# Kernel optimization log

Measured on AMD Instinct MI355X. Metric: run time of the kernel, lower is better.

## Reference

```python
import jax, jax.numpy as jnp
import numpy as np

B, S, V, D, H, L = 4, 1024, 32000, 256, 8, 4
DH = D // H  # per-head dim (D_H == F_H since F=D)
EPS = 1e-5


def _layernorm(x, g, b):
    m = jnp.mean(x, axis=-1, keepdims=True)
    v = jnp.mean((x - m) ** 2, axis=-1, keepdims=True)
    return (x - m) * jax.lax.rsqrt(v + EPS) * g + b


def _forward(X, emb, WQ, WK, WV, O, ln_g, ln_b, w1, b1, w2, b2, w3, b3, logitW):
    x = emb[X]  # [B,S,D]
    scale = 1.0 / np.sqrt(DH).astype(np.float32)
    nlayers = WQ.shape[0]
    for i in range(nlayers):
        xn = _layernorm(x, ln_g[i], ln_b[i])
        xh = xn.reshape(B, S, H, DH)  # [B,S,H,DH]
        # repeated 'dd'/'ff' indices extract the DIAGONAL of the per-head weights
        scores = jnp.einsum('bqhd,hdd,bkhd,hdd->bhqk', xh, WQ[i], xh, WK[i]) * scale
        attn = jax.nn.softmax(scores, axis=-1)  # [B,H,S,S]
        y = jnp.einsum('bhqk,bkhf,hff->bqhf', attn, xh, WV[i]).reshape(B, S, D)
        y = jnp.einsum('bqf,ff->bqf', y, O[i])  # diagonal output scaling
        y = jax.nn.gelu(y @ w1[i] + b1[i], approximate=False)
        y = jax.nn.gelu(y @ w2[i] + b2[i], approximate=False)
        y = y @ w3[i] + b3[i]
        x = x + y
    return jnp.einsum('bqd,dt->bqt', x, logitW)  # [B,S,V]


def setup_inputs() -> dict:
    key = jax.random.key(0)
    ks = jax.random.split(key, 16)

    def xavier(k, shape, fan_in, fan_out):
        std = np.sqrt(2.0 / (fan_in + fan_out)).astype(np.float32)
        return jax.random.normal(k, shape, jnp.float32) * std

    inp = {
        'X': jax.random.randint(ks[0], (B, S), 0, V, dtype=jnp.int64),
        'emb': jax.random.normal(ks[1], (V, D), jnp.float32),
        'WQ': xavier(ks[2], (L, H, DH, DH), DH, DH),
        'WK': xavier(ks[3], (L, H, DH, DH), DH, DH),
        'WV': xavier(ks[4], (L, H, DH, DH), DH, DH),
        'O': xavier(ks[5], (L, D, D), D, D),
        'ln_g': jnp.ones((L, D), jnp.float32),
        'ln_b': jnp.zeros((L, D), jnp.float32),
        'w1': xavier(ks[6], (L, D, D), D, D),
        'b1': jnp.zeros((L, D), jnp.float32),
        'w2': xavier(ks[7], (L, D, D), D, D),
        'b2': jnp.zeros((L, D), jnp.float32),
        'w3': xavier(ks[8], (L, D, D), D, D),
        'b3': jnp.zeros((L, D), jnp.float32),
        'logitW': xavier(ks[9], (D, V), D, V),
    }
    return inp


def reference(X, emb, WQ, WK, WV, O, ln_g, ln_b, w1, b1, w2, b2, w3, b3, logitW):
    return _forward(X, emb, WQ, WK, WV, O, ln_g, ln_b, w1, b1, w2, b2, w3, b3, logitW)
```

## Files before the change

### kernel.cpp

```cpp
#include <hip/hip_runtime.h>
#include <hip/hip_bf16.h>
#include <cstdint>
#include <cstddef>

#define B_ 4
#define S_ 1024
#define V_ 32000
#define D_ 256
#define H_ 8
#define DH_ 32
#define L_ 4
#define MROWS (B_*S_)

typedef __attribute__((ext_vector_type(8))) short bf16x8;
typedef __attribute__((ext_vector_type(4))) float f32x4;

__device__ __forceinline__ unsigned short f2bf(float f) {
  union { float f; unsigned u; } c; c.f = f;
  unsigned u = c.u;
  u += 0x7fff + ((u >> 16) & 1);
  return (unsigned short)(u >> 16);
}
__device__ __forceinline__ float bf2f(unsigned short u) {
  union { unsigned u; float f; } c; c.u = ((unsigned)u) << 16; return c.f;
}

__device__ __forceinline__ void gload16(const unsigned short* g, unsigned short* l) {
  __builtin_amdgcn_global_load_lds(
      (const __attribute__((address_space(1))) void*)g,
      (__attribute__((address_space(3))) void*)l, 16, 0, 0);
}

template<int BM, int BK, int NW>
__device__ __forceinline__ void stage_tile_swz(const unsigned short* __restrict__ g, int ldg,
                                               unsigned short* lds, int wave, int lane) {
  constexpr int CH  = BM * BK * 2 / 1024;
  constexpr int BKB = BK * 2;
#pragma unroll
  for (int t = 0; t < CH / NW; ++t) {
    int c = wave + t * NW;
    int byte  = c * 1024 + lane * 16;
    int row   = byte / BKB;
    int inner = (byte % BKB) ^ ((row & 7) << 4);
    gload16(g + (size_t)row * ldg + (inner >> 1), lds + c * 512);
  }
}

template<int BKB>
__device__ __forceinline__ bf16x8 lds_frag(const unsigned short* base, int row, int kbytes) {
  int b = (row * BKB + kbytes) ^ ((row & 7) << 4);
  return *(const bf16x8*)((const char*)base + b);
}

__global__ __launch_bounds__(512) void k_prep(
    const int* __restrict__ X, const float* __restrict__ emb,
    const float* __restrict__ lng, const float* __restrict__ lnb,
    float* __restrict__ x, unsigned short* __restrict__ xbf,
    unsigned short* __restrict__ xnT,
    const float* __restrict__ w1, const float* __restrict__ w2,
    const float* __restrict__ w3, unsigned short* __restrict__ mlpW) {
  int tid = threadIdx.x;
  if (blockIdx.x < 256) {
    __shared__ __align__(16) float xf[16][264];
    __shared__ float mrow[16], rrow[16];
    int r0 = blockIdx.x * 16;
    int w = tid >> 6, lane = tid & 63;
#pragma unroll
    for (int rr = 0; rr < 2; rr++) {
      int row = w * 2 + rr; int grow = r0 + row;
      int tok = X[grow];
      f32x4 v = *(const f32x4*)(emb + (size_t)tok * D_ + lane * 4);
      *(f32x4*)(x + (size_t)grow * D_ + lane * 4) = v;
      *(f32x4*)&xf[row][lane * 4] = v;
      float s = v[0] + v[1] + v[2] + v[3];
      float ss = v[0]*v[0] + v[1]*v[1] + v[2]*v[2] + v[3]*v[3];
#pragma unroll
      for (int off = 1; off < 64; off <<= 1) {
        s  += __shfl_xor(s, off, 64);
        ss += __shfl_xor(ss, off, 64);
      }
      float mean = s * (1.f / D_);
      float var = ss * (1.f / D_) - mean * mean;
      float rinv = rsqrtf(var + 1e-5f);
      float4 g4 = *(const float4*)(lng + lane * 4);
      float4 b4 = *(const float4*)(lnb + lane * 4);
      ushort4 o;
      o.x = f2bf((v[0] - mean) * rinv * g4.x + b4.x);
      o.y = f2bf((v[1] - mean) * rinv * g4.y + b4.y);
      o.z = f2bf((v[2] - mean) * rinv * g4.z + b4.z);
      o.w = f2bf((v[3] - mean) * rinv * g4.w + b4.w);
      *(ushort4*)(xbf + (size_t)grow * D_ + lane * 4) = o;
      if (lane == 0) { mrow[row] = mean; rrow[row] = rinv; }
    }
    __syncthreads();
    int d = tid & 255, half = tid >> 8;
    float gd = lng[d], bd = lnb[d];
    int bb = r0 >> 10, s0 = r0 & 1023;
    bf16x8 o8;
#pragma unroll
    for (int k = 0; k < 8; k++) {
      int srow = half * 8 + k;
      o8[k] = (short)f2bf((xf[srow][d] - mrow[srow]) * rrow[srow] * gd + bd);
    }
    *(bf16x8*)(xnT + ((size_t)(bb * 256 + d)) * S_ + s0 + half * 8) = o8;
  } else {
    __shared__ float tile[64][65];
    int idx = blockIdx.x - 256;
    int z = idx >> 4;
    int rem = idx & 15;
    int r0 = (rem >> 2) * 64, c0 = (rem & 3) * 64;
    int l = z / 3, mm = z % 3;
    const float* in = (mm == 0 ? w1 : mm == 1 ? w2 : w3) + (size_t)l * 65536;
    unsigned short* out = mlpW + (size_t)z * 65536;
    int t = tid & 255;
    bool act = tid < 256;
    if (act) {
#pragma unroll
      for (int i = 0; i < 16; i++) {
        int id2 = i * 256 + t;
        int lr = id2 >> 6, lc = id2 & 63;
        tile[lr][lc] = in[(size_t)(r0 + lr) * 256 + c0 + lc];
      }
    }
    __syncthreads();
    if (act) {
#pragma unroll
      for (int i = 0; i < 16; i++) {
        int id2 = i * 256 + t;
        int lr = id2 >> 6, lc = id2 & 63;
        out[(size_t)(c0 + lr) * 256 + r0 + lc] = f2bf(tile[lc][lr]);
      }
    }
  }
}

template<int LAST>
__global__ __launch_bounds__(512) void k_layer(
    const unsigned short* __restrict__ xbf,
    const unsigned short* __restrict__ xnT,
    const float* __restrict__ WQ, const float* __restrict__ WK,
    const float* __restrict__ WV, const float* __restrict__ Om,
    const unsigned short* __restrict__ Wl,
    const float* __restrict__ b1, const float* __restrict__ b2, const float* __restrict__ b3,
    float* __restrict__ x,
    const float* __restrict__ lngN, const float* __restrict__ lnbN,
    unsigned short* __restrict__ xbfN, unsigned short* __restrict__ xnTN,
    unsigned short* __restrict__ actB,
    int layer) {
  __shared__ __align__(16) unsigned short P_lds[8][16][72];
  __shared__ __align__(16) unsigned short Aa[16 * 256];
  __shared__ __align__(16) unsigned short Ab[16 * 256];
  __shared__ __align__(16) unsigned short Ab2[16 * 256];
  __shared__ __align__(16) unsigned short Bp[3][256 * 64];
  __shared__ __align__(16) float xf[16][264];
  __shared__ float mrow[16], rrow[16];

  int b = blockIdx.x >> 6;
  int q0 = (blockIdx.x & 63) << 4;
  int r0 = blockIdx.x * 16;
  int tid = threadIdx.x;
  int w = tid >> 6, lane = tid & 63;
  int lr = lane & 15, lg = lane >> 4;
  int h = w;

  stage_tile_swz<256, 64, 8>(Wl, 256, Bp[0], w, lane);

  const float scale = 0.17677669529663687f;
  bf16x8 aq;
  {
    bf16x8 xq = *(const bf16x8*)(xbf + ((size_t)(b * S_ + q0 + lr)) * D_ + h * DH_ + lg * 8);
#pragma unroll
    for (int j = 0; j < 8; j++) {
      int dj = lg * 8 + j;
      float wq = WQ[((size_t)(layer * H_ + h)) * 1024 + dj * 33];
      float wk = WK[((size_t)(layer * H_ + h)) * 1024 + dj * 33];
      aq[j] = (short)f2bf(bf2f((unsigned short)xq[j]) * wq * wk * scale);
    }
  }
  float dvo[2];
#pragma unroll
  for (int fs = 0; fs < 2; fs++) {
    int fh = fs * 16 + lr;
    int fc = h * DH_ + fh;
    dvo[fs] = WV[((size_t)(layer * H_ + h)) * 1024 + fh * 33] *
              Om[(size_t)layer * 65536 + (size_t)fc * 257];
  }

  f32x4 accPV[2];
  accPV[0] = (f32x4){0.f, 0.f, 0.f, 0.f};
  accPV[1] = (f32x4){0.f, 0.f, 0.f, 0.f};
  float rsum[4] = {0.f, 0.f, 0.f, 0.f};

  const unsigned short* xk_base = xbf + ((size_t)b * S_) * D_ + h * DH_ + lg * 8;
  const unsigned short* vT_base = xnT + ((size_t)(b * D_ + h * DH_)) * S_;

  bf16x8 qkb[4];
#pragma unroll
  for (int c = 0; c < 4; c++)
    qkb[c] = *(const bf16x8*)(xk_base + (size_t)(c * 16 + lr) * D_);

  for (int kt = 0; kt < 16; kt++) {
    int k0 = kt * 64;
    bf16x8 pvb[2][2];
#pragma unroll
    for (int fs = 0; fs < 2; fs++)
#pragma unroll
      for (int kc = 0; kc < 2; kc++)
        pvb[fs][kc] = *(const bf16x8*)(vT_base + (size_t)(fs * 16 + lr) * S_ +
                                       k0 + kc * 32 + lg * 8);
    f32x4 s[4];
#pragma unroll
    for (int c = 0; c < 4; c++)
      s[c] = __builtin_amdgcn_mfma_f32_16x16x32_bf16(aq, qkb[c],
                (f32x4){0.f, 0.f, 0.f, 0.f}, 0, 0, 0);
    int ktn = kt < 15 ? kt + 1 : 15;
#pragma unroll
    for (int c = 0; c < 4; c++)
      qkb[c] = *(const bf16x8*)(xk_base + (size_t)(ktn * 64 + c * 16 + lr) * D_);
#pragma unroll
    for (int c = 0; c < 4; c++)
#pragma unroll
      for (int r = 0; r < 4; r++) {
        float p = __expf(s[c][r]);
        rsum[r] += p;
        P_lds[w][lg * 4 + r][c * 16 + lr] = f2bf(p);
      }
#pragma unroll
    for (int kc = 0; kc < 2; kc++) {
      bf16x8 pa = *(const bf16x8*)(&P_lds[w][lr][kc * 32 + lg * 8]);
#pragma unroll
      for (int fs = 0; fs < 2; fs++)
        accPV[fs] = __builtin_amdgcn_mfma_f32_16x16x32_bf16(pa, pvb[fs][kc],
                       accPV[fs], 0, 0, 0);
    }
  }

  float inv[4];
#pragma unroll
  for (int r = 0; r < 4; r++) {
    float v = rsum[r];
    v += __shfl_xor(v, 1, 64);
    v += __shfl_xor(v, 2, 64);
    v += __shfl_xor(v, 4, 64);
    v += __shfl_xor(v, 8, 64);
    inv[r] = 1.f / v;
  }
#pragma unroll
  for (int fs = 0; fs < 2; fs++)
#pragma unroll
    for (int r = 0; r < 4; r++) {
      float val = accPV[fs][r] * inv[r] * dvo[fs];
      int row = lg * 4 + r, col = h * DH_ + fs * 16 + lr;
      int byte = (row * 512 + col * 2) ^ ((row & 7) << 4);
      *(unsigned short*)((char*)Aa + byte) = f2bf(val);
    }
  __syncthreads();

  int lr16 = lr;
  f32x4 acc[2];
  acc[0] = (f32x4){0.f, 0.f, 0.f, 0.f};
  acc[1] = (f32x4){0.f, 0.f, 0.f, 0.f};
  const unsigned short* Asrc = Aa;

  stage_tile_swz<256, 64, 8>(Wl + 64, 256, Bp[1], w, lane);

  for (int p = 0; p < 12; ++p) {
    if (p < 10) {
      int pn = p + 2;
      stage_tile_swz<256, 64, 8>(Wl + (size_t)(pn >> 2) * 65536 + (pn & 3) * 64,
                                 256, Bp[pn % 3], w, lane);
    }
    int kk0 = (p & 3) * 64;
#pragma unroll
    for (int kk = 0; kk < 64; kk += 32) {
      bf16x8 a = lds_frag<512>(Asrc, lr16, (kk0 + kk) * 2 + lg * 16);
#pragma unroll
      for (int j = 0; j < 2; j++) {
        bf16x8 bfg = lds_frag<128>(Bp[p % 3], w * 32 + j * 16 + lr16, kk * 2 + lg * 16);
        acc[j] = __builtin_amdgcn_mfma_f32_16x16x32_bf16(a, bfg, acc[j], 0, 0, 0);
      }
    }
    if (p == 3 || p == 7) {
      const float* bias = (p == 3) ? b1 : b2;
      unsigned short* dst = (p == 3) ? Ab : Ab2;
#pragma unroll
      for (int j = 0; j < 2; j++) {
        int col = w * 32 + j * 16 + lr16;
        float bv = bias[col];
#pragma unroll
        for (int r = 0; r < 4; r++) {
          float v = acc[j][r] + bv;
          v = 0.5f * v * (1.f + erff(v * 0.70710678118654752f));
          int row = lg * 4 + r;
          int byte = (row * 512 + col * 2) ^ ((row & 7) << 4);
          *(unsigned short*)((char*)dst + byte) = f2bf(v);
        }
      }
      acc[0] = (f32x4){0.f, 0.f, 0.f, 0.f};
      acc[1] = (f32x4){0.f, 0.f, 0.f, 0.f};
      Asrc = (p == 3) ? Ab : Ab2;
      asm volatile("s_waitcnt lgkmcnt(0)" ::: "memory");
    }
    if (p < 10) asm volatile("s_waitcnt vmcnt(4)" ::: "memory");
    else        asm volatile("s_waitcnt vmcnt(0)" ::: "memory");
    __builtin_amdgcn_sched_barrier(0);
    __builtin_amdgcn_s_barrier();
  }

#pragma unroll
  for (int j = 0; j < 2; j++) {
    int col = w * 32 + j * 16 + lr16;
    float bv = b3[col];
#pragma unroll
    for (int r = 0; r < 4; r++) {
      int row = lg * 4 + r; int grow = r0 + row;
      float v = acc[j][r] + bv + x[(size_t)grow * D_ + col];
      if constexpr (LAST) {
        actB[(size_t)grow * D_ + col] = f2bf(v);
      } else {
        x[(size_t)grow * D_ + col] = v;
        xf[row][col] = v;
      }
    }
  }

  if constexpr (!LAST) {
    __syncthreads();
#pragma unroll
    for (int rr = 0; rr < 2; rr++) {
      int row = w * 2 + rr; int grow = r0 + row;
      f32x4 v = *(const f32x4*)&xf[row][lane * 4];
      float s = v[0] + v[1] + v[2] + v[3];
      float ss = v[0]*v[0] + v[1]*v[1] + v[2]*v[2] + v[3]*v[3];
#pragma unroll
      for (int off = 1; off < 64; off <<= 1) {
        s  += __shfl_xor(s, off, 64);
        ss += __shfl_xor(ss, off, 64);
      }
      float mean = s * (1.f / D_);
      float var = ss * (1.f / D_) - mean * mean;
      float rinv = rsqrtf(var + 1e-5f);
      float4 g4 = *(const float4*)(lngN + lane * 4);
      float4 b4 = *(const float4*)(lnbN + lane * 4);
      ushort4 o;
      o.x = f2bf((v[0] - mean) * rinv * g4.x + b4.x);
      o.y = f2bf((v[1] - mean) * rinv * g4.y + b4.y);
      o.z = f2bf((v[2] - mean) * rinv * g4.z + b4.z);
      o.w = f2bf((v[3] - mean) * rinv * g4.w + b4.w);
      *(ushort4*)(xbfN + (size_t)grow * D_ + lane * 4) = o;
      if (lane == 0) { mrow[row] = mean; rrow[row] = rinv; }
    }
    __syncthreads();
    int d = tid & 255, half = tid >> 8;
    float gd = lngN[d], bd = lnbN[d];
    int bb = r0 >> 10, s0 = r0 & 1023;
    bf16x8 o8;
#pragma unroll
    for (int k = 0; k < 8; k++) {
      int srow = half * 8 + k;
      o8[k] = (short)f2bf((xf[srow][d] - mrow[srow]) * rrow[srow] * gd + bd);
    }
    *(bf16x8*)(xnTN + ((size_t)(bb * 256 + d)) * S_ + s0 + half * 8) = o8;
  }
}

__global__ __launch_bounds__(512) void k_logits(
    const unsigned short* __restrict__ A,
    const float* __restrict__ logitW,
    float* __restrict__ C) {
  __shared__ __align__(16) unsigned short Bs[128 * 256];
  __shared__ __align__(16) unsigned short As[2][64 * 256];

  int tid = threadIdx.x, lane = tid & 63, w = tid >> 6;
  int wm = w >> 2, wn = w & 3;
  int lr = lane & 15, lg = lane >> 4;
  int bn0 = blockIdx.x * 128;

  stage_tile_swz<64, 256, 8>(A, 256, As[0], w, lane);

  {
    int c = tid & 127;
    int kp = tid >> 7;
    for (int it = 0; it < 32; ++it) {
      int k = it * 8 + kp * 2;
      float f0 = logitW[(size_t)k * V_ + bn0 + c];
      float f1 = logitW[(size_t)(k + 1) * V_ + bn0 + c];
      unsigned pack = (unsigned)f2bf(f0) | ((unsigned)f2bf(f1) << 16);
      int byte = (c * 512 + k * 2) ^ ((c & 7) << 4);
      *(unsigned*)((char*)Bs + byte) = pack;
    }
  }
  __syncthreads();

  bf16x8 breg[2][8];
#pragma unroll
  for (int j = 0; j < 2; j++)
#pragma unroll
    for (int ks = 0; ks < 8; ks++)
      breg[j][ks] = lds_frag<512>(Bs, wn * 32 + j * 16 + lr, ks * 64 + lg * 16);
  __syncthreads();

  int crr = tid >> 5, ccc = tid & 31;

  for (int t = 0; t < 64; ++t) {
    int cur = t & 1;
    char* Cs = (char*)Bs + (t & 1) * 32768;
    if (t < 63)
      stage_tile_swz<64, 256, 8>(A + (size_t)(t + 1) * 64 * 256, 256, As[cur ^ 1], w, lane);

    f32x4 acc[2][2];
#pragma unroll
    for (int i = 0; i < 2; i++)
#pragma unroll
      for (int j = 0; j < 2; j++) acc[i][j] = (f32x4){0.f, 0.f, 0.f, 0.f};

#pragma unroll
    for (int ks = 0; ks < 8; ks++) {
      bf16x8 af[2];
#pragma unroll
      for (int i = 0; i < 2; i++)
        af[i] = lds_frag<512>(As[cur], wm * 32 + i * 16 + lr, ks * 64 + lg * 16);
#pragma unroll
      for (int i = 0; i < 2; i++)
#pragma unroll
        for (int j = 0; j < 2; j++)
          acc[i][j] = __builtin_amdgcn_mfma_f32_16x16x32_bf16(breg[j][ks], af[i], acc[i][j], 0, 0, 0);
    }

#pragma unroll
    for (int i = 0; i < 2; i++)
#pragma unroll
      for (int j = 0; j < 2; j++) {
        int row = wm * 32 + i * 16 + lr;
        int byte = (row * 512 + (wn * 32 + j * 16 + lg * 4) * 4) ^ ((row & 7) << 4);
        *(f32x4*)(Cs + byte) = acc[i][j];
      }

    asm volatile("s_waitcnt vmcnt(4) lgkmcnt(0)" ::: "memory");
    __builtin_amdgcn_sched_barrier(0);
    __builtin_amdgcn_s_barrier();

    int r0 = t * 64;
#pragma unroll
    for (int pss = 0; pss < 4; ++pss) {
      int row = pss * 16 + crr;
      int byte = (row * 512 + ccc * 16) ^ ((row & 7) << 4);
      f32x4 v = *(const f32x4*)(Cs + byte);
      __builtin_nontemporal_store(v, (f32x4*)(C + (size_t)(r0 + row) * V_ + bn0 + ccc * 4));
    }
  }
}

extern "C" void kernel_launch(void* const* d_in, const int* in_sizes, int n_in,
                              void* d_out, int out_size, void* d_ws, size_t ws_size,
                              hipStream_t stream) {
  const int*   X      = (const int*)d_in[0];
  const float* emb    = (const float*)d_in[1];
  const float* WQ     = (const float*)d_in[2];
  const float* WK     = (const float*)d_in[3];
  const float* WV     = (const float*)d_in[4];
  const float* Om     = (const float*)d_in[5];
  const float* lng    = (const float*)d_in[6];
  const float* lnb    = (const float*)d_in[7];
  const float* w1     = (const float*)d_in[8];
  const float* b1     = (const float*)d_in[9];
  const float* w2     = (const float*)d_in[10];
  const float* b2     = (const float*)d_in[11];
  const float* w3     = (const float*)d_in[12];
  const float* b3     = (const float*)d_in[13];
  const float* logitW = (const float*)d_in[14];
  float* out = (float*)d_out;
  char* ws = (char*)d_ws;

  constexpr size_t MB = 1024u * 1024;
  float* x  = (float*)(ws);
  unsigned short* xbf0 = (unsigned short*)(ws + 4 * MB);
  unsigned short* xbf1 = (unsigned short*)(ws + 6 * MB);
  unsigned short* xnT0 = (unsigned short*)(ws + 8 * MB);
  unsigned short* xnT1 = (unsigned short*)(ws + 10 * MB);
  unsigned short* actB = (unsigned short*)(ws + 12 * MB);
  unsigned short* mlpW = (unsigned short*)(ws + 14 * MB);

  k_prep<<<448, 512, 0, stream>>>(X, emb, lng, lnb, x, xbf0, xnT0, w1, w2, w3, mlpW);

  for (int l = 0; l < L_; l++) {
    const unsigned short* xbfI = (l & 1) ? xbf1 : xbf0;
    const unsigned short* xnTI = (l & 1) ? xnT1 : xnT0;
    unsigned short* xbfO = (l & 1) ? xbf0 : xbf1;
    unsigned short* xnTO = (l & 1) ? xnT0 : xnT1;
    if (l < L_ - 1) {
      k_layer<0><<<256, 512, 0, stream>>>(
          xbfI, xnTI, WQ, WK, WV, Om, mlpW + (size_t)(l * 3) * 65536,
          b1 + (size_t)l * D_, b2 + (size_t)l * D_, b3 + (size_t)l * D_, x,
          lng + (size_t)(l + 1) * D_, lnb + (size_t)(l + 1) * D_,
          xbfO, xnTO, nullptr, l);
    } else {
      k_layer<1><<<256, 512, 0, stream>>>(
          xbfI, xnTI, WQ, WK, WV, Om, mlpW + (size_t)(l * 3) * 65536,
          b1 + (size_t)l * D_, b2 + (size_t)l * D_, b3 + (size_t)l * D_, x,
          nullptr, nullptr, nullptr, nullptr, actB, l);
    }
  }

  k_logits<<<250, 512, 0, stream>>>(actB, logitW, out);
}
```

Baseline: 296.8 us.

## Stage MLP weight slices per-wave to drop per-step block barriers

Each wave now loads only the 32 weight columns it consumes into the triple-buffered LDS tiles, so the MLP loop no longer needs a block-wide barrier every step. Per-wave vmcnt waits now gate buffer reuse, and barriers remain only at the layer transitions where activations are shared. Bias values for the three MLP layers are preloaded into registers up front. The risk is correctness: there is no longer a barrier before a wave overwrites a buffer, so the change relies on each wave touching only its own slice, and the initial weight prefetch now starts later, after attention.

Measured after the change: 290.7 us. 1.02x faster.

```diff
diff --git a/kernel.cpp b/kernel.cpp
--- a/kernel.cpp
+++ b/kernel.cpp
@@ -163,8 +163,6 @@
   int lr = lane & 15, lg = lane >> 4;
   int h = w;
 
-  stage_tile_swz<256, 64, 8>(Wl, 256, Bp[0], w, lane);
-
   const float scale = 0.17677669529663687f;
   bf16x8 aq;
   {
@@ -184,6 +182,12 @@
     int fc = h * DH_ + fh;
     dvo[fs] = WV[((size_t)(layer * H_ + h)) * 1024 + fh * 33] *
               Om[(size_t)layer * 65536 + (size_t)fc * 257];
+  }
+  float bv1[2], bv2[2], bv3[2];
+#pragma unroll
+  for (int j = 0; j < 2; j++) {
+    int col = w * 32 + j * 16 + lr;
+    bv1[j] = b1[col]; bv2[j] = b2[col]; bv3[j] = b3[col];
   }
 
   f32x4 accPV[2];
@@ -262,14 +266,34 @@
   acc[1] = (f32x4){0.f, 0.f, 0.f, 0.f};
   const unsigned short* Asrc = Aa;
 
-  stage_tile_swz<256, 64, 8>(Wl + 64, 256, Bp[1], w, lane);
+#define STAGE_OWN(PN, BUF)                                                        \
+  {                                                                               \
+    const unsigned short* gsrc = Wl + (size_t)((PN) >> 2) * 65536 + ((PN) & 3) * 64; \
+    _Pragma("unroll")                                                             \
+    for (int tt = 0; tt < 4; ++tt) {                                              \
+      int c = w * 4 + tt;                                                         \
+      int byteo = c * 1024 + lane * 16;                                           \
+      int row = byteo >> 7;                                                       \
+      int inner = (byteo & 127) ^ ((row & 7) << 4);                               \
+      gload16(gsrc + (size_t)row * 256 + (inner >> 1), (BUF) + c * 512);          \
+    }                                                                             \
+  }
+
+  STAGE_OWN(0, Bp[0])
+  STAGE_OWN(1, Bp[1])
 
   for (int p = 0; p < 12; ++p) {
     if (p < 10) {
       int pn = p + 2;
-      stage_tile_swz<256, 64, 8>(Wl + (size_t)(pn >> 2) * 65536 + (pn & 3) * 64,
-                                 256, Bp[pn % 3], w, lane);
-    }
+      STAGE_OWN(pn, Bp[pn % 3])
+      asm volatile("s_waitcnt vmcnt(8)" ::: "memory");
+    } else if (p == 10) {
+      asm volatile("s_waitcnt vmcnt(4)" ::: "memory");
+    } else {
+      asm volatile("s_waitcnt vmcnt(0)" ::: "memory");
+    }
+    __builtin_amdgcn_sched_barrier(0);
+
     int kk0 = (p & 3) * 64;
 #pragma unroll
     for (int kk = 0; kk < 64; kk += 32) {
@@ -281,12 +305,12 @@
       }
     }
     if (p == 3 || p == 7) {
-      const float* bias = (p == 3) ? b1 : b2;
+      const float* bvp = (p == 3) ? bv1 : bv2;
       unsigned short* dst = (p == 3) ? Ab : Ab2;
 #pragma unroll
       for (int j = 0; j < 2; j++) {
         int col = w * 32 + j * 16 + lr16;
-        float bv = bias[col];
+        float bv = bvp[j];
 #pragma unroll
         for (int r = 0; r < 4; r++) {
           float v = acc[j][r] + bv;
@@ -300,17 +324,15 @@
       acc[1] = (f32x4){0.f, 0.f, 0.f, 0.f};
       Asrc = (p == 3) ? Ab : Ab2;
       asm volatile("s_waitcnt lgkmcnt(0)" ::: "memory");
-    }
-    if (p < 10) asm volatile("s_waitcnt vmcnt(4)" ::: "memory");
-    else        asm volatile("s_waitcnt vmcnt(0)" ::: "memory");
-    __builtin_amdgcn_sched_barrier(0);
-    __builtin_amdgcn_s_barrier();
+      __builtin_amdgcn_sched_barrier(0);
+      __builtin_amdgcn_s_barrier();
+    }
   }
 
 #pragma unroll
   for (int j = 0; j < 2; j++) {
     int col = w * 32 + j * 16 + lr16;
-    float bv = b3[col];
+    float bv = bv3[j];
 #pragma unroll
     for (int r = 0; r < 4; r++) {
       int row = lg * 4 + r; int grow = r0 + row;
@@ -362,6 +384,7 @@
     }
     *(bf16x8*)(xnTN + ((size_t)(bb * 256 + d)) * S_ + s0 + half * 8) = o8;
   }
+#undef STAGE_OWN
 }
 
 __global__ __launch_bounds__(512) void k_logits(
```
